# Kernel optimization log

Measured on AMD Instinct MI355X. Metric: run time of the kernel, lower is better.

## Reference

```python
import jax, jax.numpy as jnp
import numpy as np

B, H, W, C = 4, 16, 16, 1024
D_INNER, D_STATE, DT_RANK, K = 2048, 32, 64, 4
NTXT = 4096
L = H * W


def _selective_scan(u, dt, A, Bs, Cs, Ds):
    # u, dt: (B,K,D,L); A: (K,D,N); Bs, Cs: (B,K,N,L); Ds: (K,D)
    u_l = jnp.moveaxis(u, -1, 0)
    dt_l = jnp.moveaxis(dt, -1, 0)
    B_l = jnp.moveaxis(Bs, -1, 0)
    C_l = jnp.moveaxis(Cs, -1, 0)
    h0 = jnp.zeros(u.shape[:3] + (A.shape[-1],), u.dtype)

    def step(h, xs):
        u_t, dt_t, B_t, C_t = xs
        dA = jnp.exp(dt_t[..., None] * A)                    # (B,K,D,N)
        h = h * dA + dt_t[..., None] * B_t[:, :, None, :] * u_t[..., None]
        y = jnp.einsum('bkdn,bkn->bkd', h, C_t)
        return h, y

    _, ys = jax.lax.scan(step, h0, (u_l, dt_l, B_l, C_l))
    return jnp.moveaxis(ys, 0, -1) + Ds[None, :, :, None] * u


def _forward(image_embeds, text_embeds, in_proj_w, conv_w, conv_b, x_proj_w,
             dt_proj_w, dt_proj_b, A_logs, Ds, out_norm_w, out_norm_b, out_proj_w):
    b = image_embeds.shape[0]
    # in_proj -> split into x (scanned) and z (gate)
    xz = jnp.einsum('bhwc,ec->bhwe', image_embeds, in_proj_w)    # (B,H,W,2*D_INNER)
    x, z = jnp.split(xz, 2, axis=-1)
    # depthwise conv 3x3 + SiLU
    xc = jnp.transpose(x, (0, 3, 1, 2))                          # (B,D,H,W)
    xc = jax.lax.conv_general_dilated(xc, conv_w, (1, 1), 'SAME',
                                      feature_group_count=D_INNER,
                                      dimension_numbers=('NCHW', 'OIHW', 'NCHW'))
    xc = jax.nn.silu(xc + conv_b[None, :, None, None])
    # cross-scan: row-major, col-major, and their reverses
    xm = xc.reshape(b, D_INNER, L)
    xt = jnp.transpose(xc, (0, 1, 3, 2)).reshape(b, D_INNER, L)
    xs = jnp.stack([xm, xt, xm[..., ::-1], xt[..., ::-1]], axis=1)  # (B,4,D,L)
    # low-rank input-dependent params
    x_dbl = jnp.einsum('bkdl,kcd->bkcl', xs, x_proj_w)
    dts, Bmat, Cmat = jnp.split(x_dbl, [DT_RANK, DT_RANK + D_STATE], axis=2)
    dts = jnp.einsum('bkrl,kdr->bkdl', dts, dt_proj_w)
    dts = jax.nn.softplus(dts + dt_proj_b[None, :, :, None])
    A = -jnp.exp(A_logs).reshape(K, D_INNER, D_STATE)
    ys = _selective_scan(xs, dts, A, Bmat, Cmat, Ds.reshape(K, D_INNER))
    # cross-merge
    y = ys[:, 0] + ys[:, 2, :, ::-1]
    y_col = ys[:, 1] + ys[:, 3, :, ::-1]
    y = y + jnp.transpose(y_col.reshape(b, D_INNER, W, H), (0, 1, 3, 2)).reshape(b, D_INNER, L)
    # out_norm (LayerNorm over channels) + gate + out_proj
    y = jnp.transpose(y, (0, 2, 1))                              # (B,L,D)
    mu = y.mean(-1, keepdims=True)
    var = ((y - mu) ** 2).mean(-1, keepdims=True)
    y = (y - mu) * jax.lax.rsqrt(var + 1e-5) * out_norm_w + out_norm_b
    y = y.reshape(b, H, W, D_INNER) * jax.nn.silu(z)
    enhanced = jnp.einsum('bhwd,cd->bhwc', y, out_proj_w)        # (B,H,W,C)
    # L2 normalize + similarity logits
    img = enhanced / jnp.linalg.norm(enhanced, axis=-1, keepdims=True)
    txt = text_embeds / jnp.linalg.norm(text_embeds, axis=-1, keepdims=True)
    return jnp.matmul(img, txt.T)                                # (B,H,W,NTXT)


def setup_inputs() -> dict:
    key = jax.random.key(0)
    ks = jax.random.split(key, 8)
    s = 0.02
    return dict(
        image_embeds=jax.random.normal(ks[0], (B, H, W, C), jnp.float32),
        text_embeds=jax.random.normal(ks[1], (NTXT, C), jnp.float32),
        in_proj_w=jax.random.normal(ks[2], (2 * D_INNER, C), jnp.float32) * s,
        conv_w=jax.random.normal(ks[3], (D_INNER, 1, 3, 3), jnp.float32) * s,
        conv_b=jnp.zeros((D_INNER,), jnp.float32),
        x_proj_w=jax.random.normal(ks[4], (K, DT_RANK + 2 * D_STATE, D_INNER), jnp.float32) * s,
        dt_proj_w=jax.random.normal(ks[5], (K, D_INNER, DT_RANK), jnp.float32) * s,
        dt_proj_b=jax.random.normal(ks[6], (K, D_INNER), jnp.float32) * s,
        A_logs=jnp.log(jnp.broadcast_to(jnp.arange(1, D_STATE + 1, dtype=jnp.float32), (K * D_INNER, D_STATE)).copy()),
        Ds=jnp.ones((K * D_INNER,), jnp.float32),
        out_norm_w=jnp.ones((D_INNER,), jnp.float32),
        out_norm_b=jnp.zeros((D_INNER,), jnp.float32),
        out_proj_w=jax.random.normal(ks[7], (C, D_INNER), jnp.float32) * s,
    )


def reference(image_embeds, text_embeds, in_proj_w, conv_w, conv_b, x_proj_w,
              dt_proj_w, dt_proj_b, A_logs, Ds, out_norm_w, out_norm_b, out_proj_w):
    return _forward(image_embeds, text_embeds, in_proj_w, conv_w, conv_b, x_proj_w,
                    dt_proj_w, dt_proj_b, A_logs, Ds, out_norm_w, out_norm_b, out_proj_w)
```

## Files before the change

kernel.cpp:

```cpp
#include <hip/hip_runtime.h>
#include <math.h>


typedef unsigned short u16;
typedef __attribute__((ext_vector_type(8))) short short8;
typedef __attribute__((ext_vector_type(8))) unsigned short ushort8;
typedef __attribute__((ext_vector_type(4))) float f32x4;

__device__ __forceinline__ float sigmoidf_(float x) { return 1.f / (1.f + __expf(-x)); }

__device__ __forceinline__ u16 f2bf(float x) {
  unsigned u = __float_as_uint(x);
  unsigned r = u + 0x7FFFu + ((u >> 16) & 1u);
  return (u16)(r >> 16);
}
__device__ __forceinline__ float bf2f(u16 h) { return __uint_as_float((unsigned)h << 16); }

__device__ __forceinline__ void gl_lds16(const u16* g, u16* l) {
  __builtin_amdgcn_global_load_lds((__attribute__((address_space(1))) void*)g,
                                   (__attribute__((address_space(3))) void*)l, 16, 0, 0);
}

__global__ __launch_bounds__(256) void cvt_swz(
    const float* __restrict__ in, u16* __restrict__ hi, u16* __restrict__ lo,
    int R, int bpr , int lda)
{
  long t = (long)blockIdx.x * 256 + threadIdx.x;
  if (t >= (long)R * bpr) return;
  int m = (int)(t / bpr);
  int rb = (int)(t - (long)m * bpr);
  int kc = rb >> 2, g = rb & 3;
  const float* src = in + (long)m * lda + (kc << 5) + (g << 2);
  float4 a = *(const float4*)src;
  float4 b = *(const float4*)(src + 16);
  float v[8] = {a.x, a.y, a.z, a.w, b.x, b.y, b.z, b.w};
  ushort8 H, L;
#pragma unroll
  for (int q = 0; q < 8; q++) {
    u16 h = f2bf(v[q]);
    H[q] = h;
    L[q] = f2bf(v[q] - bf2f(h));
  }
  long off = (((long)kc * R + m) << 5) + ((long)((g ^ ((m >> 1) & 3)) << 3));
  *(ushort8*)(hi + off) = H;
  *(ushort8*)(lo + off) = L;
}

__global__ __launch_bounds__(256) void mfma_nt(
    const u16* __restrict__ Ahi, const u16* __restrict__ Alo,
    const u16* __restrict__ Bhi, const u16* __restrict__ Blo,
    float* __restrict__ C, int Mtot, int Ntot, int Ksteps, int ldc,
    int sArows, int sBrows, int bmod, long sC, long sCk, int ksplit)
{
  __shared__ u16 smem[16384];
  const int tid = threadIdx.x, lane = tid & 63, wid = tid >> 6;
  const int zb = blockIdx.z / ksplit, zk = blockIdx.z - zb * ksplit;
  const int m0 = blockIdx.y << 7, n0 = blockIdx.x << 7;

  const u16* sg;
  long row0;
  int tot;
  if (wid < 2) { row0 = (long)zb * sArows + m0; tot = Mtot; sg = wid ? Alo : Ahi; }
  else         { row0 = (long)(zb % bmod) * sBrows + n0; tot = Ntot; sg = (wid == 3) ? Blo : Bhi; }
  u16* sl = smem + (wid << 12);
  const int laneoff = lane << 3;

  f32x4 acc[4][4];
#pragma unroll
  for (int i = 0; i < 4; i++)
#pragma unroll
    for (int j = 0; j < 4; j++) acc[i][j] = (f32x4)0.f;

  const int wr = wid >> 1, wc = wid & 1;
  const int fr = lane & 15, g = lane >> 4;
  int offA[4], offB[4];
#pragma unroll
  for (int i = 0; i < 4; i++) {
    int rA = wr * 64 + i * 16 + fr;
    offA[i] = rA * 32 + ((g ^ ((rA >> 1) & 3)) << 3);
    int rB = wc * 64 + i * 16 + fr;
    offB[i] = rB * 32 + ((g ^ ((rB >> 1) & 3)) << 3);
  }

  for (int kc = 0; kc < Ksteps; ++kc) {
    const int kcg = zk * Ksteps + kc;
    const u16* s = sg + ((long)kcg * tot + row0) * 32 + laneoff;
#pragma unroll
    for (int c = 0; c < 8; ++c) gl_lds16(s + c * 512, sl + c * 512 + laneoff);
    asm volatile("s_waitcnt vmcnt(0)" ::: "memory");
    __syncthreads();

    short8 ah[4], al[4], bh[4], bl[4];
#pragma unroll
    for (int i = 0; i < 4; i++) {
      ah[i] = *(const short8*)(smem + offA[i]);
      al[i] = *(const short8*)(smem + 4096 + offA[i]);
      bh[i] = *(const short8*)(smem + 8192 + offB[i]);
      bl[i] = *(const short8*)(smem + 12288 + offB[i]);
    }
#pragma unroll
    for (int i = 0; i < 4; i++)
#pragma unroll
      for (int j = 0; j < 4; j++) {
        acc[i][j] = __builtin_amdgcn_mfma_f32_16x16x32_bf16(ah[i], bh[j], acc[i][j], 0, 0, 0);
        acc[i][j] = __builtin_amdgcn_mfma_f32_16x16x32_bf16(ah[i], bl[j], acc[i][j], 0, 0, 0);
        acc[i][j] = __builtin_amdgcn_mfma_f32_16x16x32_bf16(al[i], bh[j], acc[i][j], 0, 0, 0);
      }
    __syncthreads();
  }

  float* Cb = C + (long)zb * sC + (long)zk * sCk;
  const int r0 = m0 + wr * 64, c0 = n0 + wc * 64;
#pragma unroll
  for (int i = 0; i < 4; i++)
#pragma unroll
    for (int j = 0; j < 4; j++) {
      const long cc = c0 + j * 16 + fr;
#pragma unroll
      for (int q = 0; q < 4; q++)
        Cb[(long)(r0 + i * 16 + g * 4 + q) * ldc + cc] = acc[i][j][q];
    }
}

__global__ __launch_bounds__(256) void sum8(float* __restrict__ px)
{
  long t = (long)blockIdx.x * 256 + threadIdx.x;
  if (t >= 524288) return;
  float s = px[t];
#pragma unroll
  for (int p = 1; p < 8; p++) s += px[(long)p * 524288 + t];
  px[t] = s;
}

__global__ __launch_bounds__(256) void zero_buf(float4* __restrict__ p)
{
  p[(long)blockIdx.x * 256 + threadIdx.x] = (float4){0.f, 0.f, 0.f, 0.f};
}

__global__ __launch_bounds__(256) void conv_scatter_bf16(
    const float* __restrict__ xz, const float* __restrict__ cw,
    const float* __restrict__ cb, u16* __restrict__ hi, u16* __restrict__ lo)
{
  const int p = blockIdx.x & 255;
  const int b = blockIdx.x >> 8;
  const int h = p >> 4, w = p & 15;
  const int l1 = (w << 4) + h;
  const int pos[4] = {p, l1, 255 - p, 255 - l1};
#pragma unroll
  for (int it = 0; it < 8; it++) {
    const int d = it * 256 + threadIdx.x;
    float acc = cb[d];
#pragma unroll
    for (int dh = 0; dh < 3; dh++) {
      const int hh = h + dh - 1;
      if (hh < 0 || hh > 15) continue;
#pragma unroll
      for (int dw = 0; dw < 3; dw++) {
        const int ww = w + dw - 1;
        if (ww < 0 || ww > 15) continue;
        acc = fmaf(xz[((long)(b * 256 + (hh << 4) + ww)) * 4096 + d],
                   cw[d * 9 + dh * 3 + dw], acc);
      }
    }
    const float sv = acc * sigmoidf_(acc);
    const u16 hv = f2bf(sv);
    const u16 lv = f2bf(sv - bf2f(hv));
    const int kc = d >> 5, dd = d & 31;
    const int g0 = (dd < 16) ? (dd >> 2) : ((dd - 16) >> 2);
    const int slot = (dd < 16) ? (dd & 3) : 4 + ((dd - 16) & 3);
#pragma unroll
    for (int kk = 0; kk < 4; kk++) {
      const int m = (b * 4 + kk) * 256 + pos[kk];
      const long off = (((long)kc * 4096 + m) << 5) + ((g0 ^ ((m >> 1) & 3)) << 3) + slot;
      hi[off] = hv;
      lo[off] = lv;
    }
  }
}

__global__ __launch_bounds__(256) void scan_fused(
    const u16* __restrict__ xs_hi, const u16* __restrict__ xs_lo,
    const float* __restrict__ xdbl, const float* __restrict__ w_dt,
    const float* __restrict__ b_dt, const float* __restrict__ A_logs,
    const float* __restrict__ Dsv, float* __restrict__ ym)
{
  const int tid = threadIdx.x;
  const int k = blockIdx.y, b = blockIdx.z;
  const int bk = b * 4 + k;
  const int dbase = blockIdx.x << 6;
  const int mbase = bk * 256;
  const int kc0 = dbase >> 5;

  const int dc = tid >> 2, sub = tid & 3;
  const int d = dbase + dc;
  const int kd = k * 2048 + d;
  const int n0 = sub * 8;

  float a[8], hst[8];
#pragma unroll
  for (int j = 0; j < 8; j++) {
    a[j] = -__expf(A_logs[(long)kd * 32 + n0 + j]);
    hst[j] = 0.f;
  }
  const float Dval = Dsv[kd];
  const long obase = (long)b * 256 * 2048 + d;

  const int lam = tid & 63, wv = tid >> 6;
  const int kdd = k * 2048 + dbase + lam;
  float wdt[64];
  const float* wp = w_dt + (long)kdd * 64;
#pragma unroll
  for (int c = 0; c < 64; c += 4) *(float4*)&wdt[c] = *(const float4*)(wp + c);
  const float bdt = b_dt[kdd];

  const float* xb = xdbl + (long)bk * 256 * 128;

  __shared__ float xd[32][128];
  __shared__ float dtS[32][64];
  __shared__ float uS[32][64];

  for (int l0 = 0; l0 < 256; l0 += 32) {
    __syncthreads();
#pragma unroll
    for (int i = 0; i < 4; i++) {
      const int idx = i * 256 + tid;
      const int r = idx >> 5, c = idx & 31;
      *(float4*)&xd[r][c * 4] = *(const float4*)(xb + (l0 + r) * 128 + c * 4);
    }
    {
      const int r = tid >> 3, kcl = (tid >> 2) & 1, part = tid & 3;
      const int m = mbase + l0 + r;
      const long go = (((long)(kc0 + kcl) * 4096 + m) << 5) + part * 8;
      const ushort8 Hv = *(const ushort8*)(xs_hi + go);
      const ushort8 Lv = *(const ushort8*)(xs_lo + go);
      const int gx = part ^ ((m >> 1) & 3);
      float lo4[4], hi4[4];
#pragma unroll
      for (int q = 0; q < 4; q++) {
        lo4[q] = bf2f(Hv[q]) + bf2f(Lv[q]);
        hi4[q] = bf2f(Hv[4 + q]) + bf2f(Lv[4 + q]);
      }
      *(float4*)&uS[r][kcl * 32 + gx * 4] = *(float4*)lo4;
      *(float4*)&uS[r][kcl * 32 + 16 + gx * 4] = *(float4*)hi4;
    }
    __syncthreads();
#pragma unroll
    for (int s = 0; s < 8; s++) {
      const int ls = wv * 8 + s;
      float acc = 0.f;
#pragma unroll
      for (int c4 = 0; c4 < 16; c4++) {
        const float4 xv = *(const float4*)&xd[ls][c4 * 4];
        acc = fmaf(wdt[c4 * 4 + 0], xv.x, acc);
        acc = fmaf(wdt[c4 * 4 + 1], xv.y, acc);
        acc = fmaf(wdt[c4 * 4 + 2], xv.z, acc);
        acc = fmaf(wdt[c4 * 4 + 3], xv.w, acc);
      }
      const float xsp = acc + bdt;
      dtS[ls][lam] = (xsp > 20.f) ? xsp : log1pf(__expf(xsp));
    }
    __syncthreads();
#pragma unroll 4
    for (int ls = 0; ls < 32; ls++) {
      const int l = l0 + ls;
      const float dt = dtS[ls][dc];
      const float u = uS[ls][dc];
      const float dtu = dt * u;
      float y = 0.f;
#pragma unroll
      for (int j = 0; j < 8; j++) {
        const float dA = __expf(a[j] * dt);
        hst[j] = fmaf(hst[j], dA, dtu * xd[ls][64 + n0 + j]);
        y = fmaf(hst[j], xd[ls][96 + n0 + j], y);
      }
      y += __shfl_xor(y, 1);
      y += __shfl_xor(y, 2);
      if (sub == 0) {
        int p;
        if (k == 0) p = l;
        else if (k == 1) p = ((l & 15) << 4) + (l >> 4);
        else if (k == 2) p = 255 - l;
        else { const int lr = 255 - l; p = ((lr & 15) << 4) + (lr >> 4); }
        atomicAdd(&ym[obase + (long)p * 2048], fmaf(Dval, u, y));
      }
    }
  }
}

__global__ __launch_bounds__(256) void ln_gate_cvt(
    const float* __restrict__ ym, const float* __restrict__ xz,
    const float* __restrict__ lw, const float* __restrict__ lb,
    u16* __restrict__ hi, u16* __restrict__ lo)
{
  const int row = blockIdx.x;
  const int tid = threadIdx.x;
  const float* yr = ym + (long)row * 2048;

  __shared__ float sg[2048];
  __shared__ float sm[8];
  float v[8];
  float s = 0.f, ss = 0.f;
#pragma unroll
  for (int i = 0; i < 8; i++) {
    const float t = yr[i * 256 + tid];
    v[i] = t;
    s += t;
    ss += t * t;
  }
#pragma unroll
  for (int off = 32; off > 0; off >>= 1) {
    s += __shfl_down(s, off);
    ss += __shfl_down(ss, off);
  }
  const int lane = tid & 63, wid = tid >> 6;
  if (lane == 0) { sm[wid] = s; sm[4 + wid] = ss; }
  __syncthreads();
  const float S = sm[0] + sm[1] + sm[2] + sm[3];
  const float SS = sm[4] + sm[5] + sm[6] + sm[7];
  const float mu = S * (1.f / 2048.f);
  const float var = SS * (1.f / 2048.f) - mu * mu;
  const float inv = rsqrtf(var + 1e-5f);
#pragma unroll
  for (int i = 0; i < 8; i++) {
    const int d = i * 256 + tid;
    const float yn = (v[i] - mu) * inv * lw[d] + lb[d];
    const float zz = xz[(long)row * 4096 + 2048 + d];
    sg[d] = yn * zz * sigmoidf_(zz);
  }
  __syncthreads();
  const int kc = tid >> 2, g = tid & 3;
  const int c0 = kc * 32 + g * 4;
  ushort8 H, L;
#pragma unroll
  for (int q = 0; q < 4; q++) {
    const float f0 = sg[c0 + q], f1 = sg[c0 + 16 + q];
    const u16 h0 = f2bf(f0), h1 = f2bf(f1);
    H[q] = h0; H[4 + q] = h1;
    L[q] = f2bf(f0 - bf2f(h0));
    L[4 + q] = f2bf(f1 - bf2f(h1));
  }
  const long off = (((long)kc * 1024 + row) << 5) + ((long)((g ^ ((row >> 1) & 3)) << 3));
  *(ushort8*)(hi + off) = H;
  *(ushort8*)(lo + off) = L;
}

template <int P>
__global__ __launch_bounds__(256) void l2cvt(
    const float* __restrict__ in, long pstride,
    u16* __restrict__ hi, u16* __restrict__ lo, int R)
{
  const int row = blockIdx.x;
  const int tid = threadIdx.x;
  __shared__ float sg[1024];
  __shared__ float sm[4];
  float ss = 0.f;
  for (int i = tid; i < 1024; i += 256) {
    float v = in[(long)row * 1024 + i];
#pragma unroll
    for (int p2 = 1; p2 < P; p2++) v += in[(long)p2 * pstride + (long)row * 1024 + i];
    sg[i] = v;
    ss += v * v;
  }
#pragma unroll
  for (int off = 32; off > 0; off >>= 1) ss += __shfl_down(ss, off);
  const int lane = tid & 63, wid = tid >> 6;
  if (lane == 0) sm[wid] = ss;
  __syncthreads();
  const float sc = rsqrtf(sm[0] + sm[1] + sm[2] + sm[3]);
  if (tid < 128) {
    const int kc = tid >> 2, g = tid & 3;
    const int c0 = kc * 32 + g * 4;
    ushort8 H, L;
#pragma unroll
    for (int q = 0; q < 4; q++) {
      const float f0 = sg[c0 + q] * sc, f1 = sg[c0 + 16 + q] * sc;
      const u16 h0 = f2bf(f0), h1 = f2bf(f1);
      H[q] = h0; H[4 + q] = h1;
      L[q] = f2bf(f0 - bf2f(h0));
      L[4 + q] = f2bf(f1 - bf2f(h1));
    }
    const long off = (((long)kc * R + row) << 5) + ((long)((g ^ ((row >> 1) & 3)) << 3));
    *(ushort8*)(hi + off) = H;
    *(ushort8*)(lo + off) = L;
  }
}

extern "C" void kernel_launch(void* const* d_in, const int* in_sizes, int n_in,
                              void* d_out, int out_size, void* d_ws, size_t ws_size,
                              hipStream_t stream)
{
  const float* img = (const float*)d_in[0];
  const float* txt = (const float*)d_in[1];
  const float* w_in = (const float*)d_in[2];
  const float* conv_w = (const float*)d_in[3];
  const float* conv_b = (const float*)d_in[4];
  const float* w_x = (const float*)d_in[5];
  const float* w_dt = (const float*)d_in[6];
  const float* b_dt = (const float*)d_in[7];
  const float* A_logs = (const float*)d_in[8];
  const float* Dsv = (const float*)d_in[9];
  const float* ln_w = (const float*)d_in[10];
  const float* ln_b = (const float*)d_in[11];
  const float* w_out = (const float*)d_in[12];
  float* out = (float*)d_out;

  float* ws = (float*)d_ws;
  float* xz = ws;
  float* Cr = ws + 4194304;
  u16* imgsw_h = (u16*)Cr;
  u16* imgsw_l = (u16*)(Cr + 524288);
  u16* w_insw_h = (u16*)(Cr + 1048576);
  u16* w_insw_l = (u16*)(Cr + 3145728);
  u16* xs_hi = (u16*)Cr;
  u16* xs_lo = (u16*)(Cr + 4194304);
  u16* outgsw_h = (u16*)Cr;
  u16* outgsw_l = (u16*)(Cr + 1048576);
  u16* w_outsw_h = (u16*)(Cr + 2097152);
  u16* w_outsw_l = (u16*)(Cr + 3145728);
  u16* enhsw_h = (u16*)(Cr + 4194304);
  u16* enhsw_l = (u16*)(Cr + 4718592);
  u16* w_xsw_h = (u16*)(ws + 12582912);
  u16* w_xsw_l = (u16*)(ws + 13107200);
  float* ym = ws + 13631488;
  u16* txtnsw_h = (u16*)xz;
  u16* txtnsw_l = (u16*)(xz + 2097152);

  float* ob = (float*)d_out;
  float* px8 = ob;
  float* xdbl = px8;
  float* px4 = ob;

  cvt_swz<<<512, 256, 0, stream>>>(img, imgsw_h, imgsw_l, 1024, 128, 1024);
  cvt_swz<<<2048, 256, 0, stream>>>(w_in, w_insw_h, w_insw_l, 4096, 128, 1024);
  cvt_swz<<<512, 256, 0, stream>>>(w_x, w_xsw_h, w_xsw_l, 512, 256, 2048);

  mfma_nt<<<dim3(32, 8, 1), 256, 0, stream>>>(imgsw_h, imgsw_l, w_insw_h, w_insw_l,
                                              xz, 1024, 4096, 32, 4096, 0, 0, 1, 0, 0, 1);

  conv_scatter_bf16<<<dim3(1024), 256, 0, stream>>>(xz, conv_w, conv_b, xs_hi, xs_lo);

  mfma_nt<<<dim3(1, 2, 128), 256, 0, stream>>>(xs_hi, xs_lo, w_xsw_h, w_xsw_l,
                                               px8, 4096, 512, 8, 128, 256, 128, 4,
                                               32768, 524288, 8);
  sum8<<<2048, 256, 0, stream>>>(px8);
  zero_buf<<<2048, 256, 0, stream>>>((float4*)ym);

  scan_fused<<<dim3(32, 4, 4), 256, 0, stream>>>(xs_hi, xs_lo, xdbl, w_dt, b_dt,
                                                 A_logs, Dsv, ym);

  ln_gate_cvt<<<dim3(1024), 256, 0, stream>>>(ym, xz, ln_w, ln_b, outgsw_h, outgsw_l);

  cvt_swz<<<1024, 256, 0, stream>>>(w_out, w_outsw_h, w_outsw_l, 1024, 256, 2048);

  mfma_nt<<<dim3(8, 8, 4), 256, 0, stream>>>(outgsw_h, outgsw_l, w_outsw_h, w_outsw_l,
                                             px4, 1024, 1024, 16, 1024, 0, 0, 1,
                                             0, 1048576, 4);

  l2cvt<4><<<dim3(1024), 256, 0, stream>>>(px4, 1048576, enhsw_h, enhsw_l, 1024);
  l2cvt<1><<<dim3(4096), 256, 0, stream>>>(txt, 0, txtnsw_h, txtnsw_l, 4096);

  mfma_nt<<<dim3(32, 8, 1), 256, 0, stream>>>(enhsw_h, enhsw_l, txtnsw_h, txtnsw_l,
                                              out, 1024, 4096, 32, 4096, 0, 0, 1, 0, 0, 1);
}
```

Before: 434.4 us.

## Vectorize conv scatter stores via LDS and split scan state across 8 lanes

The depthwise conv kernel now stages SiLU outputs in a rotated shared-memory buffer. Each thread then gathers eight channels and writes 16-byte ushort8 stores into the swizzled hi/lo layout, replacing scattered 2-byte stores. The selective scan kernel moves to 512 threads per block, so each channel's 32 states are split over 8 lanes of 4 states instead of 4 lanes of 8. This doubles in-flight parallelism and shortens each thread's serial recurrence, at the cost of one extra shuffle reduction step and more threads contending on LDS.

```diff
diff --git a/kernel.cpp b/kernel.cpp
--- a/kernel.cpp
+++ b/kernel.cpp
@@ -146,6 +146,7 @@
   const int h = p >> 4, w = p & 15;
   const int l1 = (w << 4) + h;
   const int pos[4] = {p, l1, 255 - p, 255 - l1};
+  __shared__ float sg[2048];
 #pragma unroll
   for (int it = 0; it < 8; it++) {
     const int d = it * 256 + threadIdx.x;
@@ -163,22 +164,32 @@
       }
     }
     const float sv = acc * sigmoidf_(acc);
-    const u16 hv = f2bf(sv);
-    const u16 lv = f2bf(sv - bf2f(hv));
-    const int kc = d >> 5, dd = d & 31;
-    const int g0 = (dd < 16) ? (dd >> 2) : ((dd - 16) >> 2);
-    const int slot = (dd < 16) ? (dd & 3) : 4 + ((dd - 16) & 3);
-#pragma unroll
-    for (int kk = 0; kk < 4; kk++) {
-      const int m = (b * 4 + kk) * 256 + pos[kk];
-      const long off = (((long)kc * 4096 + m) << 5) + ((g0 ^ ((m >> 1) & 3)) << 3) + slot;
-      hi[off] = hv;
-      lo[off] = lv;
-    }
-  }
-}
-
-__global__ __launch_bounds__(256) void scan_fused(
+    const int kc = d >> 5, x = d & 31;
+    sg[kc * 32 + ((x + kc) & 31)] = sv;
+  }
+  __syncthreads();
+  const int kc = threadIdx.x >> 2, g = threadIdx.x & 3;
+  ushort8 H, L;
+#pragma unroll
+  for (int q = 0; q < 4; q++) {
+    const int x0 = g * 4 + q;
+    const float f0 = sg[kc * 32 + ((x0 + kc) & 31)];
+    const float f1 = sg[kc * 32 + ((x0 + 16 + kc) & 31)];
+    const u16 h0 = f2bf(f0), h1 = f2bf(f1);
+    H[q] = h0; H[4 + q] = h1;
+    L[q] = f2bf(f0 - bf2f(h0));
+    L[4 + q] = f2bf(f1 - bf2f(h1));
+  }
+#pragma unroll
+  for (int kk = 0; kk < 4; kk++) {
+    const int m = (b * 4 + kk) * 256 + pos[kk];
+    const long off = (((long)kc * 4096 + m) << 5) + ((g ^ ((m >> 1) & 3)) << 3);
+    *(ushort8*)(hi + off) = H;
+    *(ushort8*)(lo + off) = L;
+  }
+}
+
+__global__ __launch_bounds__(512, 4) void scan_fused(
     const u16* __restrict__ xs_hi, const u16* __restrict__ xs_lo,
     const float* __restrict__ xdbl, const float* __restrict__ w_dt,
     const float* __restrict__ b_dt, const float* __restrict__ A_logs,
@@ -191,14 +202,14 @@
   const int mbase = bk * 256;
   const int kc0 = dbase >> 5;
 
-  const int dc = tid >> 2, sub = tid & 3;
+  const int dc = tid >> 3, sub = tid & 7;
   const int d = dbase + dc;
   const int kd = k * 2048 + d;
-  const int n0 = sub * 8;
-
-  float a[8], hst[8];
-#pragma unroll
-  for (int j = 0; j < 8; j++) {
+  const int n0 = sub * 4;
+
+  float a[4], hst[4];
+#pragma unroll
+  for (int j = 0; j < 4; j++) {
     a[j] = -__expf(A_logs[(long)kd * 32 + n0 + j]);
     hst[j] = 0.f;
   }
@@ -222,12 +233,12 @@
   for (int l0 = 0; l0 < 256; l0 += 32) {
     __syncthreads();
 #pragma unroll
-    for (int i = 0; i < 4; i++) {
-      const int idx = i * 256 + tid;
+    for (int i = 0; i < 2; i++) {
+      const int idx = i * 512 + tid;
       const int r = idx >> 5, c = idx & 31;
       *(float4*)&xd[r][c * 4] = *(const float4*)(xb + (l0 + r) * 128 + c * 4);
     }
-    {
+    if (tid < 256) {
       const int r = tid >> 3, kcl = (tid >> 2) & 1, part = tid & 3;
       const int m = mbase + l0 + r;
       const long go = (((long)(kc0 + kcl) * 4096 + m) << 5) + part * 8;
@@ -245,8 +256,8 @@
     }
     __syncthreads();
 #pragma unroll
-    for (int s = 0; s < 8; s++) {
-      const int ls = wv * 8 + s;
+    for (int s = 0; s < 4; s++) {
+      const int ls = wv * 4 + s;
       float acc = 0.f;
 #pragma unroll
       for (int c4 = 0; c4 < 16; c4++) {
@@ -266,15 +277,20 @@
       const float dt = dtS[ls][dc];
       const float u = uS[ls][dc];
       const float dtu = dt * u;
+      const float4 Bv = *(const float4*)&xd[ls][64 + n0];
+      const float4 Cv = *(const float4*)&xd[ls][96 + n0];
       float y = 0.f;
 #pragma unroll
-      for (int j = 0; j < 8; j++) {
+      for (int j = 0; j < 4; j++) {
         const float dA = __expf(a[j] * dt);
-        hst[j] = fmaf(hst[j], dA, dtu * xd[ls][64 + n0 + j]);
-        y = fmaf(hst[j], xd[ls][96 + n0 + j], y);
+        const float bj = (j == 0) ? Bv.x : (j == 1) ? Bv.y : (j == 2) ? Bv.z : Bv.w;
+        const float cj = (j == 0) ? Cv.x : (j == 1) ? Cv.y : (j == 2) ? Cv.z : Cv.w;
+        hst[j] = fmaf(hst[j], dA, dtu * bj);
+        y = fmaf(hst[j], cj, y);
       }
       y += __shfl_xor(y, 1);
       y += __shfl_xor(y, 2);
+      y += __shfl_xor(y, 4);
       if (sub == 0) {
         int p;
         if (k == 0) p = l;
@@ -445,7 +461,7 @@
   sum8<<<2048, 256, 0, stream>>>(px8);
   zero_buf<<<2048, 256, 0, stream>>>((float4*)ym);
 
-  scan_fused<<<dim3(32, 4, 4), 256, 0, stream>>>(xs_hi, xs_lo, xdbl, w_dt, b_dt,
+  scan_fused<<<dim3(32, 4, 4), 512, 0, stream>>>(xs_hi, xs_lo, xdbl, w_dt, b_dt,
                                                  A_logs, Dsv, ym);
 
   ln_gate_cvt<<<dim3(1024), 256, 0, stream>>>(ym, xz, ln_w, ln_b, outgsw_h, outgsw_l);
```

Measured after the change: 437.4 us. About the same (+0.7%).
